# Kernel optimization log

Hardware: AMD Instinct MI355X
Metric: run time of the kernel (lower is better)

## Reference

```python
import jax, jax.numpy as jnp
import numpy as np

N, D, NF = 65536, 512, 32  # samples, flattened dim, n_transformations


def setup_inputs() -> dict:
    key = jax.random.key(0)
    k1, k2, k3, k4 = jax.random.split(key, 4)
    lim = float(np.sqrt(1.0 / D))  # reset_parameters uniform bound
    x = jax.random.normal(k1, (N, D), dtype=jnp.float32)
    u = jax.random.uniform(k2, (NF, D), dtype=jnp.float32, minval=-lim, maxval=lim)
    w = jax.random.uniform(k3, (NF, D), dtype=jnp.float32, minval=-lim, maxval=lim)
    b = jax.random.uniform(k4, (NF,), dtype=jnp.float32, minval=-lim, maxval=lim)
    return {"x": x, "u": u, "w": w, "b": b}


def reference(x, u, w, b):
    """Chain of NF planar flows (nn.Sequential of SinglePlanarFlow).
    Returns (transformed samples [N,D], summed log|det J| per sample [N])."""

    def step(xc, params):
        ui, wi, bi = params  # [D], [D], scalar
        wtu = jnp.dot(wi, ui)
        m_wtu = -1.0 + jnp.log1p(jnp.exp(wtu))
        # enforce invertibility: u_hat = u + (m(wtu)-wtu) * w / ||w||^2 when wtu < 1
        u_hat = jnp.where(wtu < 1.0, ui + (m_wtu - wtu) * wi / jnp.dot(wi, wi), ui)
        lin = xc @ wi + bi          # [N]
        t = jnp.tanh(lin)           # h(lin)
        out = xc + t[:, None] * u_hat
        # psi @ u_hat^T = h'(lin) * (w . u_hat)
        logdet = jnp.log(jnp.abs(1.0 + (1.0 - t * t) * jnp.dot(wi, u_hat)))  # [N]
        return out, logdet

    out, logdets = jax.lax.scan(step, x, (u, w, b))  # logdets: [NF, N]
    return out, jnp.sum(logdets, axis=0)
```

## Files before the change

kernel.cpp:

```cpp
#include <hip/hip_runtime.h>
#include <math.h>

#define NS 65536
#define DD 512
#define NF 32

__global__ __launch_bounds__(256) void k_uhat(const float* __restrict__ u,
                                              const float* __restrict__ w,
                                              float* __restrict__ u_hat) {
    const int i = blockIdx.x;
    const int tid = threadIdx.x;
    __shared__ float s_wu[256];
    __shared__ float s_ww[256];
    float pu = 0.f, pw = 0.f;
    for (int d = tid; d < DD; d += 256) {
        float wv = w[i * DD + d];
        pu += wv * u[i * DD + d];
        pw += wv * wv;
    }
    s_wu[tid] = pu;
    s_ww[tid] = pw;
    __syncthreads();
    for (int s = 128; s > 0; s >>= 1) {
        if (tid < s) {
            s_wu[tid] += s_wu[tid + s];
            s_ww[tid] += s_ww[tid + s];
        }
        __syncthreads();
    }
    const float wtu = s_wu[0];
    const float ww  = s_ww[0];
    float scale = 0.f;
    if (wtu < 1.f) {
        float m = -1.f + log1pf(expf(wtu));
        scale = (m - wtu) / ww;
    }
    for (int d = tid; d < DD; d += 256) {
        u_hat[i * DD + d] = u[i * DD + d] + scale * w[i * DD + d];
    }
}

__global__ __launch_bounds__(256) void k_gmat(const float* __restrict__ u_hat,
                                              const float* __restrict__ w,
                                              float* __restrict__ G) {
    const int tid = blockIdx.x * 256 + threadIdx.x;
    const int i = tid >> 5;
    const int j = tid & 31;
    const float* uh = u_hat + i * DD;
    const float* wj = w + j * DD;
    float s = 0.f;
    for (int d = 0; d < DD; ++d) s += uh[d] * wj[d];
    G[i * NF + j] = s;
}

#define KC 64

__global__ __launch_bounds__(256) void k_lin(const float* __restrict__ x,
                                             const float* __restrict__ w,
                                             float* __restrict__ LT) {
    __shared__ float xs[64 * KC];
    const int t  = threadIdx.x;
    const int jg = __builtin_amdgcn_readfirstlane(t >> 6);
    const int rl = t & 63;
    const int r0 = blockIdx.x * 64;

    float acc[8];
#pragma unroll
    for (int jj = 0; jj < 8; ++jj) acc[jj] = 0.f;

    for (int kc = 0; kc < DD; kc += KC) {
        __syncthreads();
#pragma unroll
        for (int i = 0; i < 4; ++i) {
            const int f   = i * 256 + t;
            const int row = f >> 4;
            const int c4  = f & 15;
            const float4 v = *(const float4*)(x + (size_t)(r0 + row) * DD + kc + c4 * 4);
            const int byte = row * 256 + ((c4 * 16) ^ ((row & 7) << 4));
            *(float4*)((char*)xs + byte) = v;
        }
        __syncthreads();
#pragma unroll
        for (int c4 = 0; c4 < 16; ++c4) {
            const int byte = rl * 256 + ((c4 * 16) ^ ((rl & 7) << 4));
            const float4 xv = *(const float4*)((const char*)xs + byte);
#pragma unroll
            for (int jj = 0; jj < 8; ++jj) {
                const float* wp = w + (size_t)(jg * 8 + jj) * DD + kc + c4 * 4;
                acc[jj] += xv.x * wp[0] + xv.y * wp[1] + xv.z * wp[2] + xv.w * wp[3];
            }
        }
    }
    float* lp = LT + (size_t)(r0 + rl) * NF + jg * 8;
    *(float4*)(lp)     = make_float4(acc[0], acc[1], acc[2], acc[3]);
    *(float4*)(lp + 4) = make_float4(acc[4], acc[5], acc[6], acc[7]);
}

__global__ __launch_bounds__(256) void k_rec(float* __restrict__ LT,
                                             const float* __restrict__ b,
                                             const float* __restrict__ G,
                                             float* __restrict__ logdet) {
    const int r = blockIdx.x * 256 + threadIdx.x;
    float* lp = LT + (size_t)r * NF;

    float lin[NF];
#pragma unroll
    for (int j = 0; j < NF; j += 4) {
        float4 v = *(const float4*)(lp + j);
        lin[j] = v.x + b[j]; lin[j+1] = v.y + b[j+1];
        lin[j+2] = v.z + b[j+2]; lin[j+3] = v.w + b[j+3];
    }

    float ldet = 0.f;
#pragma unroll
    for (int j = 0; j < NF; ++j) {
        const float tt = tanhf(lin[j]);
        const float gd = G[j * NF + j];
        ldet += logf(fabsf(1.f + (1.f - tt * tt) * gd));
#pragma unroll
        for (int i = j + 1; i < NF; ++i) lin[i] = fmaf(tt, G[j * NF + i], lin[i]);
        lin[j] = tt;
    }

#pragma unroll
    for (int j = 0; j < NF; j += 4) {
        *(float4*)(lp + j) = make_float4(lin[j], lin[j+1], lin[j+2], lin[j+3]);
    }
    logdet[r] = ldet;
}

#define OUT_R 32

__global__ __launch_bounds__(256) void k_out(const float* __restrict__ x,
                                             const float* __restrict__ u_hat,
                                             const float* __restrict__ T,
                                             float* __restrict__ out) {
    const int wid  = __builtin_amdgcn_readfirstlane(blockIdx.x * 4 + (threadIdx.x >> 6));
    const int lane = threadIdx.x & 63;
    const int cg   = wid & 1;
    const int rg   = wid >> 1;
    const int col  = cg * 256 + lane * 4;

    float4 uh[NF];
#pragma unroll
    for (int j = 0; j < NF; ++j) uh[j] = *(const float4*)(u_hat + (size_t)j * DD + col);

    for (int rr = 0; rr < OUT_R; ++rr) {
        const int r = rg * OUT_R + rr;
        float4 o = *(const float4*)(x + (size_t)r * DD + col);
#pragma unroll
        for (int j = 0; j < NF; ++j) {
            const float tj = T[(size_t)r * NF + j];
            o.x = fmaf(tj, uh[j].x, o.x);
            o.y = fmaf(tj, uh[j].y, o.y);
            o.z = fmaf(tj, uh[j].z, o.z);
            o.w = fmaf(tj, uh[j].w, o.w);
        }
        *(float4*)(out + (size_t)r * DD + col) = o;
    }
}

__global__ __launch_bounds__(256) void k_flow(const float* __restrict__ x,
                                              const float* __restrict__ w,
                                              const float* __restrict__ b,
                                              const float* __restrict__ u_hat,
                                              const float* __restrict__ G,
                                              float* __restrict__ out,
                                              float* __restrict__ logdet) {
    const int r = blockIdx.x * 256 + threadIdx.x;
    const float* xr = x + (size_t)r * DD;
    float lin[NF];
#pragma unroll
    for (int j = 0; j < NF; ++j) lin[j] = b[j];
    for (int c = 0; c < DD; c += 16) {
        const float4 x0 = *(const float4*)(xr + c);
        const float4 x1 = *(const float4*)(xr + c + 4);
        const float4 x2 = *(const float4*)(xr + c + 8);
        const float4 x3 = *(const float4*)(xr + c + 12);
#pragma unroll
        for (int j = 0; j < NF; ++j) {
            const float* wj = w + j * DD + c;
            float acc;
            acc  = x0.x * wj[0]  + x0.y * wj[1]  + x0.z * wj[2]  + x0.w * wj[3];
            acc += x1.x * wj[4]  + x1.y * wj[5]  + x1.z * wj[6]  + x1.w * wj[7];
            acc += x2.x * wj[8]  + x2.y * wj[9]  + x2.z * wj[10] + x2.w * wj[11];
            acc += x3.x * wj[12] + x3.y * wj[13] + x3.z * wj[14] + x3.w * wj[15];
            lin[j] += acc;
        }
    }
    float ldet = 0.f;
#pragma unroll
    for (int j = 0; j < NF; ++j) {
        const float t = tanhf(lin[j]);
        const float det = 1.f + (1.f - t * t) * G[j * NF + j];
        ldet += logf(fabsf(det));
#pragma unroll
        for (int i = j + 1; i < NF; ++i) lin[i] += t * G[j * NF + i];
        lin[j] = t;
    }
    float* outr = out + (size_t)r * DD;
    for (int c = 0; c < DD; c += 8) {
        float4 a0 = *(const float4*)(xr + c);
        float4 a1 = *(const float4*)(xr + c + 4);
#pragma unroll
        for (int j = 0; j < NF; ++j) {
            const float* uj = u_hat + j * DD + c;
            const float t = lin[j];
            a0.x += t * uj[0]; a0.y += t * uj[1]; a0.z += t * uj[2]; a0.w += t * uj[3];
            a1.x += t * uj[4]; a1.y += t * uj[5]; a1.z += t * uj[6]; a1.w += t * uj[7];
        }
        *(float4*)(outr + c)     = a0;
        *(float4*)(outr + c + 4) = a1;
    }
    logdet[r] = ldet;
}

extern "C" void kernel_launch(void* const* d_in, const int* in_sizes, int n_in,
                              void* d_out, int out_size, void* d_ws, size_t ws_size,
                              hipStream_t stream) {
    const float* x = (const float*)d_in[0];
    const float* u = (const float*)d_in[1];
    const float* w = (const float*)d_in[2];
    const float* b = (const float*)d_in[3];

    float* out    = (float*)d_out;
    float* logdet = out + (size_t)NS * DD;

    float* u_hat = (float*)d_ws;
    float* G     = u_hat + NF * DD;
    float* LT    = G + NF * NF;

    const size_t need = (size_t)(NF * DD + NF * NF + (size_t)NS * NF) * sizeof(float);

    k_uhat<<<NF, 256, 0, stream>>>(u, w, u_hat);
    k_gmat<<<(NF * NF) / 256, 256, 0, stream>>>(u_hat, w, G);

    if (ws_size >= need) {
        k_lin<<<NS / 64, 256, 0, stream>>>(x, w, LT);
        k_rec<<<NS / 256, 256, 0, stream>>>(LT, b, G, logdet);
        k_out<<<(NS / OUT_R) * 2 / 4, 256, 0, stream>>>(x, u_hat, LT, out);
    } else {
        k_flow<<<NS / 256, 256, 0, stream>>>(x, w, b, u_hat, G, out, logdet);
    }
}
```

Measured before the change: 487.3 us.

## Transpose lin buffer, prefetch x tiles in k_lin, parallelize G matrix

Switches the intermediate lin/tanh buffer from row-major [N,NF] to column-major [NF,N], so k_rec's per-thread loads and stores coalesce across threads. k_out now reads T with a stride of N per flow. k_lin adds register prefetch of the next x chunk to overlap the global load with compute, and uses explicit fma chains. k_gmat moves from one thread per dot product to one wavefront per entry with a shuffle reduction.

```diff
diff --git a/kernel.cpp b/kernel.cpp
--- a/kernel.cpp
+++ b/kernel.cpp
@@ -40,17 +40,21 @@
     }
 }
 
-__global__ __launch_bounds__(256) void k_gmat(const float* __restrict__ u_hat,
-                                              const float* __restrict__ w,
-                                              float* __restrict__ G) {
-    const int tid = blockIdx.x * 256 + threadIdx.x;
-    const int i = tid >> 5;
-    const int j = tid & 31;
-    const float* uh = u_hat + i * DD;
-    const float* wj = w + j * DD;
-    float s = 0.f;
-    for (int d = 0; d < DD; ++d) s += uh[d] * wj[d];
-    G[i * NF + j] = s;
+__global__ __launch_bounds__(64) void k_gmat(const float* __restrict__ u_hat,
+                                             const float* __restrict__ w,
+                                             float* __restrict__ G) {
+    const int i = blockIdx.x >> 5;
+    const int j = blockIdx.x & 31;
+    const int lane = threadIdx.x;
+    const float4* a = (const float4*)(u_hat + (size_t)i * DD);
+    const float4* c = (const float4*)(w + (size_t)j * DD);
+    const float4 a0 = a[lane],      c0 = c[lane];
+    const float4 a1 = a[lane + 64], c1 = c[lane + 64];
+    float s = a0.x * c0.x + a0.y * c0.y + a0.z * c0.z + a0.w * c0.w
+            + a1.x * c1.x + a1.y * c1.y + a1.z * c1.z + a1.w * c1.w;
+#pragma unroll
+    for (int off = 32; off > 0; off >>= 1) s += __shfl_xor(s, off);
+    if (lane == 0) G[i * NF + j] = s;
 }
 
 #define KC 64
@@ -64,22 +68,36 @@
     const int rl = t & 63;
     const int r0 = blockIdx.x * 64;
 
+    const int srow = t >> 4;
+    const int sc4  = t & 15;
+
     float acc[8];
 #pragma unroll
     for (int jj = 0; jj < 8; ++jj) acc[jj] = 0.f;
+
+    float4 pre[4];
+#pragma unroll
+    for (int i = 0; i < 4; ++i) {
+        const int row = (i * 256 + t) >> 4;
+        pre[i] = *(const float4*)(x + (size_t)(r0 + row) * DD + 0 + sc4 * 4);
+    }
 
     for (int kc = 0; kc < DD; kc += KC) {
         __syncthreads();
 #pragma unroll
         for (int i = 0; i < 4; ++i) {
-            const int f   = i * 256 + t;
-            const int row = f >> 4;
-            const int c4  = f & 15;
-            const float4 v = *(const float4*)(x + (size_t)(r0 + row) * DD + kc + c4 * 4);
-            const int byte = row * 256 + ((c4 * 16) ^ ((row & 7) << 4));
-            *(float4*)((char*)xs + byte) = v;
+            const int row = (i * 256 + t) >> 4;
+            const int byte = row * 256 + ((sc4 * 16) ^ ((row & 7) << 4));
+            *(float4*)((char*)xs + byte) = pre[i];
         }
         __syncthreads();
+        if (kc + KC < DD) {
+#pragma unroll
+            for (int i = 0; i < 4; ++i) {
+                const int row = (i * 256 + t) >> 4;
+                pre[i] = *(const float4*)(x + (size_t)(r0 + row) * DD + kc + KC + sc4 * 4);
+            }
+        }
 #pragma unroll
         for (int c4 = 0; c4 < 16; ++c4) {
             const int byte = rl * 256 + ((c4 * 16) ^ ((rl & 7) << 4));
@@ -87,45 +105,52 @@
 #pragma unroll
             for (int jj = 0; jj < 8; ++jj) {
                 const float* wp = w + (size_t)(jg * 8 + jj) * DD + kc + c4 * 4;
-                acc[jj] += xv.x * wp[0] + xv.y * wp[1] + xv.z * wp[2] + xv.w * wp[3];
+                acc[jj] = fmaf(xv.x, wp[0],
+                          fmaf(xv.y, wp[1],
+                          fmaf(xv.z, wp[2],
+                          fmaf(xv.w, wp[3], acc[jj]))));
             }
         }
     }
-    float* lp = LT + (size_t)(r0 + rl) * NF + jg * 8;
-    *(float4*)(lp)     = make_float4(acc[0], acc[1], acc[2], acc[3]);
-    *(float4*)(lp + 4) = make_float4(acc[4], acc[5], acc[6], acc[7]);
-}
+#pragma unroll
+    for (int jj = 0; jj < 8; ++jj)
+        LT[(size_t)(jg * 8 + jj) * NS + (r0 + rl)] = acc[jj];
+}
+
+#define REP32A(M) M(0) M(1) M(2) M(3) M(4) M(5) M(6) M(7) M(8) M(9) M(10) \
+    M(11) M(12) M(13) M(14) M(15) M(16) M(17) M(18) M(19) M(20) M(21) M(22) \
+    M(23) M(24) M(25) M(26) M(27) M(28) M(29) M(30) M(31)
+#define REP32B(M) M(0) M(1) M(2) M(3) M(4) M(5) M(6) M(7) M(8) M(9) M(10) \
+    M(11) M(12) M(13) M(14) M(15) M(16) M(17) M(18) M(19) M(20) M(21) M(22) \
+    M(23) M(24) M(25) M(26) M(27) M(28) M(29) M(30) M(31)
 
 __global__ __launch_bounds__(256) void k_rec(float* __restrict__ LT,
                                              const float* __restrict__ b,
                                              const float* __restrict__ G,
                                              float* __restrict__ logdet) {
     const int r = blockIdx.x * 256 + threadIdx.x;
-    float* lp = LT + (size_t)r * NF;
-
-    float lin[NF];
-#pragma unroll
-    for (int j = 0; j < NF; j += 4) {
-        float4 v = *(const float4*)(lp + j);
-        lin[j] = v.x + b[j]; lin[j+1] = v.y + b[j+1];
-        lin[j+2] = v.z + b[j+2]; lin[j+3] = v.w + b[j+3];
-    }
+
+#define DECLL(I) float l##I = LT[(size_t)(I) * NS + r] + b[I];
+    REP32A(DECLL)
+#undef DECLL
 
     float ldet = 0.f;
-#pragma unroll
-    for (int j = 0; j < NF; ++j) {
-        const float tt = tanhf(lin[j]);
-        const float gd = G[j * NF + j];
-        ldet += logf(fabsf(1.f + (1.f - tt * tt) * gd));
-#pragma unroll
-        for (int i = j + 1; i < NF; ++i) lin[i] = fmaf(tt, G[j * NF + i], lin[i]);
-        lin[j] = tt;
-    }
-
-#pragma unroll
-    for (int j = 0; j < NF; j += 4) {
-        *(float4*)(lp + j) = make_float4(lin[j], lin[j+1], lin[j+2], lin[j+3]);
-    }
+#define UPD(I) l##I = fmaf(((I) > JJ) ? tt : 0.0f, gr[I], l##I);
+#define STEP(J) { \
+        const float tt = tanhf(l##J); \
+        const float* gr = G + (J) * NF; \
+        ldet += logf(fabsf(fmaf(1.f - tt * tt, gr[J], 1.f))); \
+        const int JJ = (J); \
+        REP32B(UPD) \
+        l##J = tt; \
+    }
+    REP32A(STEP)
+#undef STEP
+#undef UPD
+
+#define STOREL(I) LT[(size_t)(I) * NS + r] = l##I;
+    REP32A(STOREL)
+#undef STOREL
     logdet[r] = ldet;
 }
 
@@ -150,7 +175,7 @@
         float4 o = *(const float4*)(x + (size_t)r * DD + col);
 #pragma unroll
         for (int j = 0; j < NF; ++j) {
-            const float tj = T[(size_t)r * NF + j];
+            const float tj = T[(size_t)j * NS + r];
             o.x = fmaf(tj, uh[j].x, o.x);
             o.y = fmaf(tj, uh[j].y, o.y);
             o.z = fmaf(tj, uh[j].z, o.z);
@@ -233,7 +258,7 @@
     const size_t need = (size_t)(NF * DD + NF * NF + (size_t)NS * NF) * sizeof(float);
 
     k_uhat<<<NF, 256, 0, stream>>>(u, w, u_hat);
-    k_gmat<<<(NF * NF) / 256, 256, 0, stream>>>(u_hat, w, G);
+    k_gmat<<<NF * NF, 64, 0, stream>>>(u_hat, w, G);
 
     if (ws_size >= need) {
         k_lin<<<NS / 64, 256, 0, stream>>>(x, w, LT);
```

Measured after the change: 517.2 us. 6.1% more time.
